# Performance work log

Hardware: AMD Instinct MI355X
Metric: run time of the kernel (lower is better)

## Reference

```python
import math
import jax, jax.numpy as jnp
import numpy as np

BSZ, N_HEADS, N_KV_HEADS, SEQLEN, HEAD_DIM = 1, 32, 8, 2048, 128
DIM = N_HEADS * HEAD_DIM  # 4096
N_REP = N_HEADS // N_KV_HEADS  # 4
NEG = -1e9


def setup_inputs() -> dict:
    key = jax.random.key(0)
    kq, kk, kv = jax.random.split(key, 3)
    q = jax.random.normal(kq, (BSZ, N_HEADS, SEQLEN, HEAD_DIM), dtype=jnp.float32)
    k = jax.random.normal(kk, (BSZ, N_KV_HEADS, SEQLEN, HEAD_DIM), dtype=jnp.float32)
    v = jax.random.normal(kv, (BSZ, N_KV_HEADS, SEQLEN, HEAD_DIM), dtype=jnp.float32)
    # additive causal mask: 0 on/below diagonal, large negative above
    causal = jnp.tril(jnp.ones((SEQLEN, SEQLEN), dtype=bool))
    mask = jnp.where(causal, 0.0, NEG).astype(jnp.float32)
    input_pos = jnp.zeros((1,), dtype=jnp.int64)
    return {"input_pos": input_pos, "q": q, "k": k, "v": v,
            "bsz": BSZ, "seqlen": SEQLEN, "mask": mask}


def reference(input_pos, q, k, v, bsz, seqlen, mask):
    # repeat_kv: (b, n_kv, s, d) -> (b, n_kv*n_rep, s, d), repeat_interleave on head dim
    k = jnp.repeat(k, N_REP, axis=1)
    v = jnp.repeat(v, N_REP, axis=1)
    scale = 1.0 / math.sqrt(q.shape[-1])
    # (b, h, s, s)
    attn = jnp.einsum("bhqd,bhkd->bhqk", q, k) * scale + mask
    attn = jax.nn.softmax(attn, axis=-1)
    y = jnp.einsum("bhqk,bhkd->bhqd", attn, v)  # (b, h, s, d)
    return y.transpose(0, 2, 1, 3).reshape(bsz, seqlen, DIM)
```

## Files before the change

### kernel.cpp

```cpp
#include <hip/hip_runtime.h>
#include <hip/hip_bf16.h>

#define SEQ 2048
#define HD 128
#define NH 32
#define NKV 8
#define ODIM 4096
#define QB 64
#define KVB 64
#define SCALE 0.08838834764831845f
#define NEGBIG -1e9f

typedef __attribute__((ext_vector_type(8))) short bf16x8;
typedef __attribute__((ext_vector_type(4))) float f32x4;

__device__ __forceinline__ unsigned short f2bf(float x) {
  union { __hip_bfloat16 b; unsigned short u; } c;
  c.b = __float2bfloat16(x);
  return c.u;
}

__device__ __forceinline__ unsigned pack2bf(float lo, float hi) {
  union { __hip_bfloat162 h; unsigned u; } c;
  c.h = __float22bfloat162_rn(float2{lo, hi});
  return c.u;
}

__global__ __launch_bounds__(512, 4) void sdpa_flash_kernel(
    const float* __restrict__ q, const float* __restrict__ k,
    const float* __restrict__ v, float* __restrict__ out) {
  __shared__ __align__(16) unsigned char smem[65536];
  const int tid = threadIdx.x;
  const int w = tid >> 6;
  const int l = tid & 63;
  const int lm = l & 15;
  const int lg = l >> 4;

  const int p = (int)blockIdx.x;
  const int qtA = p;
  const int qtB = 31 - p;
  const int myqt = (w < 4) ? qtA : qtB;
  const int h = (int)blockIdx.y;
  const int hkv = h >> 2;
  const int qbase = myqt * QB + 16 * (w & 3);
  const int myrow = qbase + lm;

  bf16x8 qa[4];
  {
    const float* qr = q + ((size_t)(h * SEQ + myrow)) * HD + 8 * lg;
    #pragma unroll
    for (int c = 0; c < 4; ++c) {
      float4 a = *(const float4*)(qr + 32 * c);
      float4 b = *(const float4*)(qr + 32 * c + 4);
      union { unsigned short hh[8]; bf16x8 vv; } pk;
      pk.hh[0] = f2bf(a.x * SCALE); pk.hh[1] = f2bf(a.y * SCALE);
      pk.hh[2] = f2bf(a.z * SCALE); pk.hh[3] = f2bf(a.w * SCALE);
      pk.hh[4] = f2bf(b.x * SCALE); pk.hh[5] = f2bf(b.y * SCALE);
      pk.hh[6] = f2bf(b.z * SCALE); pk.hh[7] = f2bf(b.w * SCALE);
      qa[c] = pk.vv;
    }
  }

  f32x4 o[8];
  #pragma unroll
  for (int i = 0; i < 8; ++i) o[i] = (f32x4){0.f, 0.f, 0.f, 0.f};
  float mrow = -1e30f;
  float lrow = 0.f;

  const int ntiles = qtB + 1;
  const float* kg0 = k + (size_t)hkv * SEQ * HD;
  const float* vg0 = v + (size_t)hkv * SEQ * HD;

  const int k_r0 = tid >> 4;
  const int k_c8 = (tid & 15) << 3;
  const int v_rr = (tid & 31) << 1;
  const int v_d0 = (tid >> 5) << 3;

  float4 ka0, kb0, ka1, kb1, va0, vb0, va1, vb1;

#define LOADT(tt) {                                                          \
    const float* kg_ = kg0 + (size_t)((tt) * KVB) * HD + k_r0 * HD + k_c8;   \
    ka0 = *(const float4*)(kg_);                                             \
    kb0 = *(const float4*)(kg_ + 4);                                         \
    ka1 = *(const float4*)(kg_ + 32 * HD);                                   \
    kb1 = *(const float4*)(kg_ + 32 * HD + 4);                               \
    const float* vg_ = vg0 + (size_t)((tt) * KVB) * HD + v_rr * HD + v_d0;   \
    va0 = *(const float4*)(vg_);                                             \
    vb0 = *(const float4*)(vg_ + 4);                                         \
    va1 = *(const float4*)(vg_ + HD);                                        \
    vb1 = *(const float4*)(vg_ + HD + 4);                                    \
  }

#define WRITELDS(bufbase) {                                                  \
    unsigned char* Kb_ = (bufbase);                                          \
    unsigned char* Vb_ = (bufbase) + 16384;                                  \
    {                                                                        \
      union { unsigned short hh[8]; uint4 u4; } pk_;                         \
      pk_.hh[0]=f2bf(ka0.x); pk_.hh[1]=f2bf(ka0.y);                          \
      pk_.hh[2]=f2bf(ka0.z); pk_.hh[3]=f2bf(ka0.w);                          \
      pk_.hh[4]=f2bf(kb0.x); pk_.hh[5]=f2bf(kb0.y);                          \
      pk_.hh[6]=f2bf(kb0.z); pk_.hh[7]=f2bf(kb0.w);                          \
      int byte_ = (k_r0 << 8) + ((k_c8 << 1) ^ ((k_r0 & 7) << 4));           \
      *(uint4*)(Kb_ + byte_) = pk_.u4;                                       \
    }                                                                        \
    {                                                                        \
      int r1_ = k_r0 + 32;                                                   \
      union { unsigned short hh[8]; uint4 u4; } pk_;                         \
      pk_.hh[0]=f2bf(ka1.x); pk_.hh[1]=f2bf(ka1.y);                          \
      pk_.hh[2]=f2bf(ka1.z); pk_.hh[3]=f2bf(ka1.w);                          \
      pk_.hh[4]=f2bf(kb1.x); pk_.hh[5]=f2bf(kb1.y);                          \
      pk_.hh[6]=f2bf(kb1.z); pk_.hh[7]=f2bf(kb1.w);                          \
      int byte_ = (r1_ << 8) + ((k_c8 << 1) ^ ((r1_ & 7) << 4));             \
      *(uint4*)(Kb_ + byte_) = pk_.u4;                                       \
    }                                                                        \
    {                                                                        \
      unsigned w0_ = pack2bf(va0.x, va1.x), w1_ = pack2bf(va0.y, va1.y);     \
      unsigned w2_ = pack2bf(va0.z, va1.z), w3_ = pack2bf(va0.w, va1.w);     \
      unsigned w4_ = pack2bf(vb0.x, vb1.x), w5_ = pack2bf(vb0.y, vb1.y);     \
      unsigned w6_ = pack2bf(vb0.z, vb1.z), w7_ = pack2bf(vb0.w, vb1.w);     \
      int rb_ = v_rr << 1;                                                   \
      int d_;                                                                \
      d_ = v_d0;     *(unsigned*)(Vb_ + (d_ << 7) + (rb_ ^ ((d_ & 7) << 4))) = w0_; \
      d_ = v_d0 + 1; *(unsigned*)(Vb_ + (d_ << 7) + (rb_ ^ ((d_ & 7) << 4))) = w1_; \
      d_ = v_d0 + 2; *(unsigned*)(Vb_ + (d_ << 7) + (rb_ ^ ((d_ & 7) << 4))) = w2_; \
      d_ = v_d0 + 3; *(unsigned*)(Vb_ + (d_ << 7) + (rb_ ^ ((d_ & 7) << 4))) = w3_; \
      d_ = v_d0 + 4; *(unsigned*)(Vb_ + (d_ << 7) + (rb_ ^ ((d_ & 7) << 4))) = w4_; \
      d_ = v_d0 + 5; *(unsigned*)(Vb_ + (d_ << 7) + (rb_ ^ ((d_ & 7) << 4))) = w5_; \
      d_ = v_d0 + 6; *(unsigned*)(Vb_ + (d_ << 7) + (rb_ ^ ((d_ & 7) << 4))) = w6_; \
      d_ = v_d0 + 7; *(unsigned*)(Vb_ + (d_ << 7) + (rb_ ^ ((d_ & 7) << 4))) = w7_; \
    }                                                                        \
  }

  LOADT(0);
  WRITELDS(smem);
  __syncthreads();
  int cur = 0;

  for (int t = 0; t < ntiles; ++t) {
    const int kv0 = t * KVB;
    const bool have_next = (t + 1 < ntiles);
    if (have_next) LOADT(t + 1);

    unsigned char* Klds = smem + (cur << 15);
    unsigned char* Vlds = Klds + 16384;

    if (t <= myqt) {
      f32x4 s[4];
      #pragma unroll
      for (int nt = 0; nt < 4; ++nt) s[nt] = (f32x4){0.f, 0.f, 0.f, 0.f};
      #pragma unroll
      for (int nt = 0; nt < 4; ++nt) {
        int r = (nt << 4) + lm;
        #pragma unroll
        for (int kc = 0; kc < 4; ++kc) {
          int byte = (r << 8) + (((kc << 6) + (lg << 4)) ^ ((r & 7) << 4));
          bf16x8 kb = *(const bf16x8*)(Klds + byte);
          s[nt] = __builtin_amdgcn_mfma_f32_16x16x32_bf16(kb, qa[kc], s[nt], 0, 0, 0);
        }
      }

      if (kv0 + KVB - 1 > qbase) {
        #pragma unroll
        for (int nt = 0; nt < 4; ++nt) {
          #pragma unroll
          for (int i = 0; i < 4; ++i) {
            int col = kv0 + (nt << 4) + (lg << 2) + i;
            s[nt][i] += (col > myrow) ? NEGBIG : 0.f;
          }
        }
      }

      float tm = -1e30f;
      #pragma unroll
      for (int nt = 0; nt < 4; ++nt)
        #pragma unroll
        for (int i = 0; i < 4; ++i) tm = fmaxf(tm, s[nt][i]);
      tm = fmaxf(tm, __shfl_xor(tm, 16));
      tm = fmaxf(tm, __shfl_xor(tm, 32));
      float mn = fmaxf(mrow, tm);
      float fac = __expf(mrow - mn);
      mrow = mn;
      float rs = 0.f;
      #pragma unroll
      for (int nt = 0; nt < 4; ++nt) {
        #pragma unroll
        for (int i = 0; i < 4; ++i) {
          float pv = __expf(s[nt][i] - mn);
          s[nt][i] = pv;
          rs += pv;
        }
      }
      rs += __shfl_xor(rs, 16);
      rs += __shfl_xor(rs, 32);
      lrow = lrow * fac + rs;
      #pragma unroll
      for (int nt2 = 0; nt2 < 8; ++nt2) {
        #pragma unroll
        for (int i = 0; i < 4; ++i) o[nt2][i] *= fac;
      }

      unsigned pk0[4], pk1[4];
      #pragma unroll
      for (int nt = 0; nt < 4; ++nt) {
        pk0[nt] = pack2bf(s[nt][0], s[nt][1]);
        pk1[nt] = pack2bf(s[nt][2], s[nt][3]);
      }
      const int srcA = lm + ((lg & 1) << 5);
      const int srcB = srcA + 16;
      const bool lo2 = (lg < 2);
      bf16x8 pb[2];
      #pragma unroll
      for (int kc = 0; kc < 2; ++kc) {
        int a0 = __shfl((int)pk0[2*kc], srcA), b0 = __shfl((int)pk0[2*kc+1], srcA);
        int a1 = __shfl((int)pk1[2*kc], srcA), b1 = __shfl((int)pk1[2*kc+1], srcA);
        int a2 = __shfl((int)pk0[2*kc], srcB), b2 = __shfl((int)pk0[2*kc+1], srcB);
        int a3 = __shfl((int)pk1[2*kc], srcB), b3 = __shfl((int)pk1[2*kc+1], srcB);
        union { int uu[4]; bf16x8 v; } pw;
        pw.uu[0] = lo2 ? a0 : b0;
        pw.uu[1] = lo2 ? a1 : b1;
        pw.uu[2] = lo2 ? a2 : b2;
        pw.uu[3] = lo2 ? a3 : b3;
        pb[kc] = pw.v;
      }

      #pragma unroll
      for (int nt2 = 0; nt2 < 8; ++nt2) {
        int dr = (nt2 << 4) + lm;
        #pragma unroll
        for (int kc = 0; kc < 2; ++kc) {
          int byte = (dr << 7) + (((kc << 6) + (lg << 4)) ^ ((dr & 7) << 4));
          bf16x8 vb = *(const bf16x8*)(Vlds + byte);
          o[nt2] = __builtin_amdgcn_mfma_f32_16x16x32_bf16(vb, pb[kc], o[nt2], 0, 0, 0);
        }
      }
    }

    if (have_next) {
      WRITELDS(smem + ((cur ^ 1) << 15));
    }
    __syncthreads();
    cur ^= 1;
  }

  float inv = 1.f / lrow;
  float* orow = out + (size_t)myrow * ODIM + h * HD + (lg << 2);
  #pragma unroll
  for (int nt2 = 0; nt2 < 8; ++nt2) {
    float4 st = {o[nt2][0] * inv, o[nt2][1] * inv, o[nt2][2] * inv, o[nt2][3] * inv};
    *(float4*)(orow + (nt2 << 4)) = st;
  }
}

extern "C" void kernel_launch(void* const* d_in, const int* in_sizes, int n_in,
                              void* d_out, int out_size, void* d_ws, size_t ws_size,
                              hipStream_t stream) {
  const float* q = (const float*)d_in[1];
  const float* k = (const float*)d_in[2];
  const float* v = (const float*)d_in[3];
  float* out = (float*)d_out;
  dim3 grid(SEQ / QB / 2, NH);
  sdpa_flash_kernel<<<grid, 512, 0, stream>>>(q, k, v, out);
}
```

Baseline: 99.70 us.

## Pre-convert K/V to swizzled bf16 tile images and stage via direct global-to-LDS loads

Adds a prepass kernel that converts K and V once into bf16 tiles already in the swizzled shared-memory layout and writes them to workspace. The main kernel then copies each tile straight into shared memory with global_load_lds, so it no longer converts and scatters K/V per block. This also halves the K/V bytes each block reads. It raises wave priority around the MFMA sections. The cost is an extra kernel launch and one pass over K/V; the old path remains as a fallback when workspace is too small.

```diff
diff --git a/kernel.cpp b/kernel.cpp
--- a/kernel.cpp
+++ b/kernel.cpp
@@ -26,9 +26,65 @@
   return c.u;
 }
 
+__device__ __forceinline__ void gload_lds16(const unsigned char* g, unsigned char* l) {
+  __builtin_amdgcn_global_load_lds(
+      (const __attribute__((address_space(1))) void*)g,
+      (__attribute__((address_space(3))) void*)l, 16, 0, 0);
+}
+
+#define KWORK (NKV * SEQ * 16)
+#define VWORK (NKV * (SEQ / 2) * 16)
+__global__ __launch_bounds__(256) void sdpa_prepass(
+    const float* __restrict__ k, const float* __restrict__ v,
+    unsigned char* __restrict__ ws) {
+  unsigned char* kimg = ws;
+  unsigned char* vimg = ws + (NKV * 32 * 16384);
+  int idx = (int)blockIdx.x * 256 + (int)threadIdx.x;
+  if (idx < KWORK) {
+    int hkv = idx >> 15;
+    int rem = idx & 32767;
+    int rg = rem >> 4;
+    int c8 = (rem & 15) << 3;
+    const float* src = k + ((size_t)hkv * SEQ + rg) * HD + c8;
+    float4 a = *(const float4*)(src);
+    float4 b = *(const float4*)(src + 4);
+    union { unsigned short hh[8]; uint4 u4; } pk;
+    pk.hh[0]=f2bf(a.x); pk.hh[1]=f2bf(a.y); pk.hh[2]=f2bf(a.z); pk.hh[3]=f2bf(a.w);
+    pk.hh[4]=f2bf(b.x); pk.hh[5]=f2bf(b.y); pk.hh[6]=f2bf(b.z); pk.hh[7]=f2bf(b.w);
+    int t = rg >> 6, r = rg & 63;
+    size_t base = ((size_t)(hkv * 32 + t)) << 14;
+    *(uint4*)(kimg + base + (r << 8) + ((c8 << 1) ^ ((r & 7) << 4))) = pk.u4;
+  } else {
+    int u = idx - KWORK;
+    if (u >= VWORK) return;
+    int hkv = u >> 14;
+    int rem = u & 16383;
+    int pr = rem >> 4;
+    int d0 = (rem & 15) << 3;
+    int rg = pr << 1;
+    const float* s0 = v + ((size_t)hkv * SEQ + rg) * HD + d0;
+    const float* s1 = s0 + HD;
+    float4 a0 = *(const float4*)(s0);
+    float4 b0 = *(const float4*)(s0 + 4);
+    float4 a1 = *(const float4*)(s1);
+    float4 b1 = *(const float4*)(s1 + 4);
+    float lo[8] = {a0.x,a0.y,a0.z,a0.w,b0.x,b0.y,b0.z,b0.w};
+    float hi[8] = {a1.x,a1.y,a1.z,a1.w,b1.x,b1.y,b1.z,b1.w};
+    int t = rg >> 6, rr = rg & 63;
+    size_t base = ((size_t)(hkv * 32 + t)) << 14;
+    int rb = rr << 1;
+    #pragma unroll
+    for (int j = 0; j < 8; ++j) {
+      int d = d0 + j;
+      *(unsigned*)(vimg + base + (d << 7) + (rb ^ ((d & 7) << 4))) =
+          pack2bf(lo[j], hi[j]);
+    }
+  }
+}
+
 __global__ __launch_bounds__(512, 4) void sdpa_flash_kernel(
-    const float* __restrict__ q, const float* __restrict__ k,
-    const float* __restrict__ v, float* __restrict__ out) {
+    const float* __restrict__ q, const unsigned char* __restrict__ kimg,
+    const unsigned char* __restrict__ vimg, float* __restrict__ out) {
   __shared__ __align__(16) unsigned char smem[65536];
   const int tid = threadIdx.x;
   const int w = tid >> 6;
@@ -68,16 +124,186 @@
   float lrow = 0.f;
 
   const int ntiles = qtB + 1;
+  const unsigned char* kt0 = kimg + (((size_t)(hkv * 32)) << 14);
+  const unsigned char* vt0 = vimg + (((size_t)(hkv * 32)) << 14);
+  const int woff = w << 10;
+
+#define STAGE(tt, bufbase) {                                                 \
+    const unsigned char* ks_ = kt0 + (((size_t)(tt)) << 14);                 \
+    const unsigned char* vs_ = vt0 + (((size_t)(tt)) << 14);                 \
+    unsigned char* Kb_ = (bufbase);                                          \
+    unsigned char* Vb_ = (bufbase) + 16384;                                  \
+    gload_lds16(ks_ + woff + (l << 4), Kb_ + woff);                          \
+    gload_lds16(ks_ + 8192 + woff + (l << 4), Kb_ + 8192 + woff);            \
+    gload_lds16(vs_ + woff + (l << 4), Vb_ + woff);                          \
+    gload_lds16(vs_ + 8192 + woff + (l << 4), Vb_ + 8192 + woff);            \
+  }
+
+  STAGE(0, smem);
+  __syncthreads();
+  int cur = 0;
+
+  for (int t = 0; t < ntiles; ++t) {
+    const int kv0 = t * KVB;
+    if (t + 1 < ntiles) STAGE(t + 1, smem + ((cur ^ 1) << 15));
+
+    unsigned char* Klds = smem + (cur << 15);
+    unsigned char* Vlds = Klds + 16384;
+
+    if (t <= myqt) {
+      f32x4 s[4];
+      #pragma unroll
+      for (int nt = 0; nt < 4; ++nt) s[nt] = (f32x4){0.f, 0.f, 0.f, 0.f};
+      __builtin_amdgcn_s_setprio(1);
+      #pragma unroll
+      for (int nt = 0; nt < 4; ++nt) {
+        int r = (nt << 4) + lm;
+        #pragma unroll
+        for (int kc = 0; kc < 4; ++kc) {
+          int byte = (r << 8) + (((kc << 6) + (lg << 4)) ^ ((r & 7) << 4));
+          bf16x8 kb = *(const bf16x8*)(Klds + byte);
+          s[nt] = __builtin_amdgcn_mfma_f32_16x16x32_bf16(kb, qa[kc], s[nt], 0, 0, 0);
+        }
+      }
+      __builtin_amdgcn_s_setprio(0);
+
+      if (kv0 + KVB - 1 > qbase) {
+        #pragma unroll
+        for (int nt = 0; nt < 4; ++nt) {
+          #pragma unroll
+          for (int i = 0; i < 4; ++i) {
+            int col = kv0 + (nt << 4) + (lg << 2) + i;
+            s[nt][i] += (col > myrow) ? NEGBIG : 0.f;
+          }
+        }
+      }
+
+      float tm = -1e30f;
+      #pragma unroll
+      for (int nt = 0; nt < 4; ++nt)
+        #pragma unroll
+        for (int i = 0; i < 4; ++i) tm = fmaxf(tm, s[nt][i]);
+      tm = fmaxf(tm, __shfl_xor(tm, 16));
+      tm = fmaxf(tm, __shfl_xor(tm, 32));
+      float mn = fmaxf(mrow, tm);
+      float fac = __expf(mrow - mn);
+      mrow = mn;
+      float rs = 0.f;
+      #pragma unroll
+      for (int nt = 0; nt < 4; ++nt) {
+        #pragma unroll
+        for (int i = 0; i < 4; ++i) {
+          float pv = __expf(s[nt][i] - mn);
+          s[nt][i] = pv;
+          rs += pv;
+        }
+      }
+      rs += __shfl_xor(rs, 16);
+      rs += __shfl_xor(rs, 32);
+      lrow = lrow * fac + rs;
+      #pragma unroll
+      for (int nt2 = 0; nt2 < 8; ++nt2) {
+        #pragma unroll
+        for (int i = 0; i < 4; ++i) o[nt2][i] *= fac;
+      }
+
+      unsigned pk0[4], pk1[4];
+      #pragma unroll
+      for (int nt = 0; nt < 4; ++nt) {
+        pk0[nt] = pack2bf(s[nt][0], s[nt][1]);
+        pk1[nt] = pack2bf(s[nt][2], s[nt][3]);
+      }
+      const int srcA = lm + ((lg & 1) << 5);
+      const int srcB = srcA + 16;
+      const bool lo2 = (lg < 2);
+      bf16x8 pb[2];
+      #pragma unroll
+      for (int kc = 0; kc < 2; ++kc) {
+        int a0 = __shfl((int)pk0[2*kc], srcA), b0 = __shfl((int)pk0[2*kc+1], srcA);
+        int a1 = __shfl((int)pk1[2*kc], srcA), b1 = __shfl((int)pk1[2*kc+1], srcA);
+        int a2 = __shfl((int)pk0[2*kc], srcB), b2 = __shfl((int)pk0[2*kc+1], srcB);
+        int a3 = __shfl((int)pk1[2*kc], srcB), b3 = __shfl((int)pk1[2*kc+1], srcB);
+        union { int uu[4]; bf16x8 v; } pw;
+        pw.uu[0] = lo2 ? a0 : b0;
+        pw.uu[1] = lo2 ? a1 : b1;
+        pw.uu[2] = lo2 ? a2 : b2;
+        pw.uu[3] = lo2 ? a3 : b3;
+        pb[kc] = pw.v;
+      }
+
+      __builtin_amdgcn_s_setprio(1);
+      #pragma unroll
+      for (int nt2 = 0; nt2 < 8; ++nt2) {
+        int dr = (nt2 << 4) + lm;
+        #pragma unroll
+        for (int kc = 0; kc < 2; ++kc) {
+          int byte = (dr << 7) + (((kc << 6) + (lg << 4)) ^ ((dr & 7) << 4));
+          bf16x8 vb = *(const bf16x8*)(Vlds + byte);
+          o[nt2] = __builtin_amdgcn_mfma_f32_16x16x32_bf16(vb, pb[kc], o[nt2], 0, 0, 0);
+        }
+      }
+      __builtin_amdgcn_s_setprio(0);
+    }
+
+    __syncthreads();
+    cur ^= 1;
+  }
+
+  float inv = 1.f / lrow;
+  float* orow = out + (size_t)myrow * ODIM + h * HD + (lg << 2);
+  #pragma unroll
+  for (int nt2 = 0; nt2 < 8; ++nt2) {
+    float4 st = {o[nt2][0] * inv, o[nt2][1] * inv, o[nt2][2] * inv, o[nt2][3] * inv};
+    *(float4*)(orow + (nt2 << 4)) = st;
+  }
+#undef STAGE
+}
+
+__global__ __launch_bounds__(512, 4) void sdpa_flash_fb(
+    const float* __restrict__ q, const float* __restrict__ k,
+    const float* __restrict__ v, float* __restrict__ out) {
+  __shared__ __align__(16) unsigned char smem[65536];
+  const int tid = threadIdx.x;
+  const int w = tid >> 6;
+  const int l = tid & 63;
+  const int lm = l & 15;
+  const int lg = l >> 4;
+  const int p = (int)blockIdx.x;
+  const int qtA = p;
+  const int qtB = 31 - p;
+  const int myqt = (w < 4) ? qtA : qtB;
+  const int h = (int)blockIdx.y;
+  const int hkv = h >> 2;
+  const int qbase = myqt * QB + 16 * (w & 3);
+  const int myrow = qbase + lm;
+  bf16x8 qa[4];
+  {
+    const float* qr = q + ((size_t)(h * SEQ + myrow)) * HD + 8 * lg;
+    #pragma unroll
+    for (int c = 0; c < 4; ++c) {
+      float4 a = *(const float4*)(qr + 32 * c);
+      float4 b = *(const float4*)(qr + 32 * c + 4);
+      union { unsigned short hh[8]; bf16x8 vv; } pk;
+      pk.hh[0] = f2bf(a.x * SCALE); pk.hh[1] = f2bf(a.y * SCALE);
+      pk.hh[2] = f2bf(a.z * SCALE); pk.hh[3] = f2bf(a.w * SCALE);
+      pk.hh[4] = f2bf(b.x * SCALE); pk.hh[5] = f2bf(b.y * SCALE);
+      pk.hh[6] = f2bf(b.z * SCALE); pk.hh[7] = f2bf(b.w * SCALE);
+      qa[c] = pk.vv;
+    }
+  }
+  f32x4 o[8];
+  #pragma unroll
+  for (int i = 0; i < 8; ++i) o[i] = (f32x4){0.f, 0.f, 0.f, 0.f};
+  float mrow = -1e30f;
+  float lrow = 0.f;
+  const int ntiles = qtB + 1;
   const float* kg0 = k + (size_t)hkv * SEQ * HD;
   const float* vg0 = v + (size_t)hkv * SEQ * HD;
-
   const int k_r0 = tid >> 4;
   const int k_c8 = (tid & 15) << 3;
   const int v_rr = (tid & 31) << 1;
   const int v_d0 = (tid >> 5) << 3;
-
   float4 ka0, kb0, ka1, kb1, va0, vb0, va1, vb1;
-
 #define LOADT(tt) {                                                          \
     const float* kg_ = kg0 + (size_t)((tt) * KVB) * HD + k_r0 * HD + k_c8;   \
     ka0 = *(const float4*)(kg_);                                             \
@@ -90,7 +316,6 @@
     va1 = *(const float4*)(vg_ + HD);                                        \
     vb1 = *(const float4*)(vg_ + HD + 4);                                    \
   }
-
 #define WRITELDS(bufbase) {                                                  \
     unsigned char* Kb_ = (bufbase);                                          \
     unsigned char* Vb_ = (bufbase) + 16384;                                  \
@@ -130,20 +355,16 @@
       d_ = v_d0 + 7; *(unsigned*)(Vb_ + (d_ << 7) + (rb_ ^ ((d_ & 7) << 4))) = w7_; \
     }                                                                        \
   }
-
   LOADT(0);
   WRITELDS(smem);
   __syncthreads();
   int cur = 0;
-
   for (int t = 0; t < ntiles; ++t) {
     const int kv0 = t * KVB;
     const bool have_next = (t + 1 < ntiles);
     if (have_next) LOADT(t + 1);
-
     unsigned char* Klds = smem + (cur << 15);
     unsigned char* Vlds = Klds + 16384;
-
     if (t <= myqt) {
       f32x4 s[4];
       #pragma unroll
@@ -158,7 +379,6 @@
           s[nt] = __builtin_amdgcn_mfma_f32_16x16x32_bf16(kb, qa[kc], s[nt], 0, 0, 0);
         }
       }
-
       if (kv0 + KVB - 1 > qbase) {
         #pragma unroll
         for (int nt = 0; nt < 4; ++nt) {
@@ -169,7 +389,6 @@
           }
         }
       }
-
       float tm = -1e30f;
       #pragma unroll
       for (int nt = 0; nt < 4; ++nt)
@@ -198,7 +417,6 @@
         #pragma unroll
         for (int i = 0; i < 4; ++i) o[nt2][i] *= fac;
       }
-
       unsigned pk0[4], pk1[4];
       #pragma unroll
       for (int nt = 0; nt < 4; ++nt) {
@@ -222,7 +440,6 @@
         pw.uu[3] = lo2 ? a3 : b3;
         pb[kc] = pw.v;
       }
-
       #pragma unroll
       for (int nt2 = 0; nt2 < 8; ++nt2) {
         int dr = (nt2 << 4) + lm;
@@ -234,14 +451,12 @@
         }
       }
     }
-
     if (have_next) {
       WRITELDS(smem + ((cur ^ 1) << 15));
     }
     __syncthreads();
     cur ^= 1;
   }
-
   float inv = 1.f / lrow;
   float* orow = out + (size_t)myrow * ODIM + h * HD + (lg << 2);
   #pragma unroll
@@ -249,6 +464,8 @@
     float4 st = {o[nt2][0] * inv, o[nt2][1] * inv, o[nt2][2] * inv, o[nt2][3] * inv};
     *(float4*)(orow + (nt2 << 4)) = st;
   }
+#undef LOADT
+#undef WRITELDS
 }
 
 extern "C" void kernel_launch(void* const* d_in, const int* in_sizes, int n_in,
@@ -259,5 +476,14 @@
   const float* v = (const float*)d_in[3];
   float* out = (float*)d_out;
   dim3 grid(SEQ / QB / 2, NH);
-  sdpa_flash_kernel<<<grid, 512, 0, stream>>>(q, k, v, out);
-}
+  const size_t need = (size_t)(NKV * 32 * 16384) * 2;
+  if (ws_size >= need && d_ws != nullptr) {
+    unsigned char* ws = (unsigned char*)d_ws;
+    int total = KWORK + VWORK;
+    sdpa_prepass<<<(total + 255) / 256, 256, 0, stream>>>(k, v, ws);
+    sdpa_flash_kernel<<<grid, 512, 0, stream>>>(
+        q, ws, ws + (NKV * 32 * 16384), out);
+  } else {
+    sdpa_flash_fb<<<grid, 512, 0, stream>>>(q, k, v, out);
+  }
+}
```

Result: faster. 86.26 us (-13.5%).
